# Optimization experiments

Measured on AMD Instinct MI355X. Metric: run time of the kernel, lower is better.

The kernel has to match this reference:

```python
import jax, jax.numpy as jnp
import numpy as np

DIM = 384
NUM_HEADS = 12
WS = 7
POSMLP_DIM = 32
HEAD_DIM = DIM // NUM_HEADS
SCALE = HEAD_DIM ** -0.5


def setup_inputs() -> dict:
    key = jax.random.key(0)
    ks = jax.random.split(key, 10)
    B_ = 2048
    N = WS * WS
    nW = 64
    inp = {
        "x": jax.random.normal(ks[0], (B_, N, DIM), dtype=jnp.float32),
        "mask": jax.random.normal(ks[1], (nW, N, N), dtype=jnp.float32),
        # qkv Linear: weight [3*dim, dim], bias [3*dim]
        "qkv_w": jax.random.normal(ks[2], (3 * DIM, DIM), dtype=jnp.float32) * (DIM ** -0.5),
        "qkv_b": jax.random.normal(ks[3], (3 * DIM,), dtype=jnp.float32) * 0.02,
        # proj Linear
        "proj_w": jax.random.normal(ks[4], (DIM, DIM), dtype=jnp.float32) * (DIM ** -0.5),
        "proj_b": jax.random.normal(ks[5], (DIM,), dtype=jnp.float32) * 0.02,
        # posmlp: Conv2d(2, posmlp_dim, 1) -> ReLU -> Conv2d(posmlp_dim, num_heads, 1)
        "pm_w1": jax.random.normal(ks[6], (POSMLP_DIM, 2), dtype=jnp.float32) * 0.5,
        "pm_b1": jax.random.normal(ks[7], (POSMLP_DIM,), dtype=jnp.float32) * 0.02,
        "pm_w2": jax.random.normal(ks[8], (NUM_HEADS, POSMLP_DIM), dtype=jnp.float32) * (POSMLP_DIM ** -0.5),
        "pm_b2": jax.random.normal(ks[9], (NUM_HEADS,), dtype=jnp.float32) * 0.02,
    }
    return inp


def _pos_bias(pm_w1, pm_b1, pm_w2, pm_b2):
    # pos_hw: [2, N] with channel 0 = row index, channel 1 = col index
    coords = jnp.arange(WS, dtype=jnp.float32)
    pos_h = jnp.repeat(coords[:, None], WS, axis=1).reshape(-1)  # row idx
    pos_w = jnp.tile(coords[None, :], (WS, 1)).reshape(-1)       # col idx
    pos = jnp.stack([pos_h, pos_w], axis=0)                      # [2, N]
    # pos_input[c, i, j] = pos[c, j] - pos[c, i]  (unsqueeze(2) - unsqueeze(3))
    d = pos[:, None, :] - pos[:, :, None]                        # [2, N, N]
    d = jnp.sign(d) * jnp.log1p(jnp.abs(d))
    # 1x1 convs == per-position channel MLP
    h = jax.nn.relu(jnp.einsum("cij,oc->oij", d, pm_w1) + pm_b1[:, None, None])
    bias = jnp.einsum("cij,oc->oij", h, pm_w2) + pm_b2[:, None, None]  # [H, N, N]
    return bias


def reference(x, mask, qkv_w, qkv_b, proj_w, proj_b, pm_w1, pm_b1, pm_w2, pm_b2):
    B_, N, C = x.shape
    H = NUM_HEADS
    qkv = x @ qkv_w.T + qkv_b                                     # [B_, N, 3C]
    qkv = qkv.reshape(B_, N, 3, H, C // H).transpose(2, 0, 3, 1, 4)
    q, k, v = qkv[0], qkv[1], qkv[2]                              # [B_, H, N, d]
    attn = jnp.einsum("bhnd,bhmd->bhnm", q * SCALE, k)            # [B_, H, N, N]
    attn = attn + _pos_bias(pm_w1, pm_b1, pm_w2, pm_b2)[None]
    nW = mask.shape[0]
    attn = attn.reshape(B_ // nW, nW, H, N, N) + mask[None, :, None]
    attn = jax.nn.softmax(attn.reshape(B_, H, N, N), axis=-1)
    out = jnp.einsum("bhnm,bhmd->bhnd", attn, v)                  # [B_, H, N, d]
    out = out.transpose(0, 2, 1, 3).reshape(B_, N, C)
    return out @ proj_w.T + proj_b
```

## Files before the change

kernel.cpp:

```cpp
#include <hip/hip_runtime.h>
#include <hip/hip_bf16.h>
#include <stdint.h>

#define DIM 384
#define QKVN 1152
#define NHEAD 12
#define HDIM 32
#define NTOK 49
#define NWIN 2048
static constexpr float SCALE_Q = 0.17677669529663687f;

typedef float f32x4 __attribute__((ext_vector_type(4)));
typedef float f32x4u __attribute__((ext_vector_type(4), aligned(4)));
typedef __bf16 bf16x8 __attribute__((ext_vector_type(8)));
typedef unsigned short u16;
typedef u16 u16x8 __attribute__((ext_vector_type(8)));
typedef u16 u16x4 __attribute__((ext_vector_type(4)));

static __device__ __forceinline__ u16 f2bf(float f) {
  __hip_bfloat16 h = __float2bfloat16(f);
  return __builtin_bit_cast(unsigned short, h);
}
static __device__ __forceinline__ f32x4 mfma_bf16(u16x8 a, u16x8 b, f32x4 c) {
  return __builtin_amdgcn_mfma_f32_16x16x32_bf16(
      __builtin_bit_cast(bf16x8, a), __builtin_bit_cast(bf16x8, b), c, 0, 0, 0);
}

__global__ void k_convert(const float* __restrict__ s, u16* __restrict__ d, int n) {
  int i = (blockIdx.x * 256 + threadIdx.x) * 4;
  if (i < n) {
    f32x4 v = *(const f32x4*)(s + i);
    u16x4 o;
    o[0] = f2bf(v[0]); o[1] = f2bf(v[1]); o[2] = f2bf(v[2]); o[3] = f2bf(v[3]);
    *(u16x4*)(d + i) = o;
  }
}

__global__ void k_posbias(const float* __restrict__ w1, const float* __restrict__ b1,
                          const float* __restrict__ w2, const float* __restrict__ b2,
                          float* __restrict__ out) {
  int idx = blockIdx.x * 256 + threadIdx.x;
  if (idx >= NTOK * NTOK) return;
  int i = idx / NTOK, j = idx % NTOK;
  float d0 = (float)(j / 7 - i / 7);
  float d1 = (float)(j % 7 - i % 7);
  d0 = copysignf(log1pf(fabsf(d0)), d0);
  d1 = copysignf(log1pf(fabsf(d1)), d1);
  float acc[NHEAD];
#pragma unroll
  for (int o2 = 0; o2 < NHEAD; o2++) acc[o2] = b2[o2];
#pragma unroll 4
  for (int o = 0; o < 32; o++) {
    float h = fmaxf(d0 * w1[o * 2] + d1 * w1[o * 2 + 1] + b1[o], 0.f);
#pragma unroll
    for (int o2 = 0; o2 < NHEAD; o2++) acc[o2] += h * w2[o2 * 32 + o];
  }
#pragma unroll
  for (int o2 = 0; o2 < NHEAD; o2++) out[(o2 * NTOK + i) * NTOK + j] = acc[o2];
}

__global__ void k_pbm(const float* __restrict__ posb, const float* __restrict__ mask,
                      float* __restrict__ pbm) {
  int idx = blockIdx.x * 256 + threadIdx.x;
  if (idx >= 64 * NHEAD * NTOK * NTOK) return;
  int j = idx % (NTOK * NTOK);
  int t = idx / (NTOK * NTOK);
  int h = t % NHEAD, w = t / NHEAD;
  pbm[idx] = posb[h * NTOK * NTOK + j] + mask[w * NTOK * NTOK + j];
}

template <int MODE>
static __device__ __forceinline__ void gemm_body(const void* __restrict__ Ap,
                                                 const u16* __restrict__ Bw,
                                                 const float* __restrict__ bias,
                                                 void* __restrict__ Cp) {
  __shared__ u16 As[2][128 * 64];
  __shared__ u16 Bs[2][128 * 64];
  const int tid = threadIdx.x;
  const int NB = (MODE == 0) ? 9 : 3;
  const int PER = (MODE == 0) ? 882 : 294;
  const int g = blockIdx.x;
  const int flat = (g & 7) * PER + (g >> 3);
  const int bm = flat / NB, bn = flat % NB;

  const int lane = tid & 63, wv = tid >> 6;
  const int wr = wv >> 1, wc = wv & 1;
  const int l15 = lane & 15, l4 = lane >> 4;
  const int sr = tid >> 1, hp = tid & 1;

  const float* a0 = (const float*)Ap + (size_t)(bm * 128 + sr) * DIM + hp * 32;
  const u16*   a1 = (const u16*)Ap + (size_t)(bm * 128 + sr) * DIM + hp * 32;
  const u16*   bb = Bw + (size_t)(bn * 128 + sr) * DIM + hp * 32;

  f32x4 fA[8];
  u16x8 rA[4], rB[4];

#define GLOAD(K0)                                                        \
  {                                                                      \
    if (MODE == 0) {                                                     \
      _Pragma("unroll") for (int i = 0; i < 8; i++)                      \
          fA[i] = *(const f32x4*)(a0 + (K0) + i * 4);                    \
    } else {                                                             \
      _Pragma("unroll") for (int i = 0; i < 4; i++)                      \
          rA[i] = *(const u16x8*)(a1 + (K0) + i * 8);                    \
    }                                                                    \
    _Pragma("unroll") for (int i = 0; i < 4; i++)                        \
        rB[i] = *(const u16x8*)(bb + (K0) + i * 8);                      \
  }

#define WLDS(BUF)                                                        \
  {                                                                      \
    _Pragma("unroll") for (int s = 0; s < 4; s++) {                      \
      u16x8 av;                                                          \
      if (MODE == 0) {                                                   \
        _Pragma("unroll") for (int j = 0; j < 4; j++) {                  \
          av[j] = f2bf(fA[2 * s][j]);                                    \
          av[j + 4] = f2bf(fA[2 * s + 1][j]);                            \
        }                                                                \
      } else av = rA[s];                                                 \
      const int st = ((hp * 4 + s) ^ (sr & 7)) * 8;                      \
      *(u16x8*)&As[BUF][sr * 64 + st] = av;                              \
      *(u16x8*)&Bs[BUF][sr * 64 + st] = rB[s];                           \
    }                                                                    \
  }

  GLOAD(0)
  WLDS(0)
  f32x4 acc[4][4] = {};

  for (int it = 0; it < 6; ++it) {
    const int cur = it & 1;
    if (it < 5) GLOAD((it + 1) * 64)
    __syncthreads();
#pragma unroll
    for (int kk = 0; kk < 2; ++kk) {
      u16x8 af[4], bfr[4];
#pragma unroll
      for (int m = 0; m < 4; m++) {
        const int row = wr * 64 + m * 16 + l15;
        af[m] = *(const u16x8*)&As[cur][row * 64 + (((kk * 4 + l4) ^ (l15 & 7)) * 8)];
      }
#pragma unroll
      for (int n = 0; n < 4; n++) {
        const int row = wc * 64 + n * 16 + l15;
        bfr[n] = *(const u16x8*)&Bs[cur][row * 64 + (((kk * 4 + l4) ^ (l15 & 7)) * 8)];
      }
#pragma unroll
      for (int m = 0; m < 4; m++)
#pragma unroll
        for (int n = 0; n < 4; n++)
          acc[m][n] = mfma_bf16(af[m], bfr[n], acc[m][n]);
    }
    if (it < 5) WLDS(cur ^ 1)
  }
#undef GLOAD
#undef WLDS

#pragma unroll
  for (int n = 0; n < 4; n++) {
    const int col = bn * 128 + wc * 64 + n * 16 + l15;
    const float bv = bias[col];
#pragma unroll
    for (int m = 0; m < 4; m++) {
      const int row0 = bm * 128 + wr * 64 + m * 16 + l4 * 4;
#pragma unroll
      for (int r = 0; r < 4; r++) {
        float v = acc[m][n][r] + bv;
        if (MODE == 0) {
          if (col < DIM) v *= SCALE_Q;
          ((u16*)Cp)[(size_t)(row0 + r) * QKVN + col] = f2bf(v);
        } else {
          ((float*)Cp)[(size_t)(row0 + r) * DIM + col] = v;
        }
      }
    }
  }
}

__global__ __launch_bounds__(256, 2) void k_qkv(const float* __restrict__ Ap,
                                                const u16* __restrict__ Bw,
                                                const float* __restrict__ bias,
                                                u16* __restrict__ Cp) {
  gemm_body<0>(Ap, Bw, bias, Cp);
}
__global__ __launch_bounds__(256, 2) void k_proj(const u16* __restrict__ Ap,
                                                 const u16* __restrict__ Bw,
                                                 const float* __restrict__ bias,
                                                 float* __restrict__ Cp) {
  gemm_body<1>(Ap, Bw, bias, Cp);
}

__global__ __launch_bounds__(256) void k_attn(const u16* __restrict__ qkv,
                                              const float* __restrict__ pbm,
                                              u16* __restrict__ aout) {
  __shared__ u16 qs[2][64 * 32];
  __shared__ u16 ks[2][64 * 32];
  __shared__ u16 vts[2][32 * 72];
  __shared__ float pbs[2][49 * 52 + 16];
  __shared__ u16 ps[64 * 72];
  const int g = blockIdx.x;
  const int b = (((g >> 3) >> 3) << 6) + (g & 7) * 8 + ((g >> 3) & 7);
  const int w = b & 63;
  const int tid = threadIdx.x;
  const int lane = tid & 63, wv = tid >> 6;
  const int l15 = lane & 15, l4 = lane >> 4;
  const int fr = (l15 >> 1) & 3;

  for (int i = tid; i < 64 * 32; i += 256)
    if ((i >> 5) >= NTOK) { qs[0][i] = 0; qs[1][i] = 0; ks[0][i] = 0; ks[1][i] = 0; }
  for (int i = tid; i < 32 * 72; i += 256)
    if ((i % 72) >= NTOK) { vts[0][i] = 0; vts[1][i] = 0; }

  const int trow = tid >> 2, tseg = tid & 3;
  const int fT = (trow >> 1) & 3;
  u16x8 rq, rk, rv;

  int psrc[3], pdst[3];
  bool pvld[3];
#pragma unroll
  for (int j = 0; j < 3; j++) {
    const int i = tid + j * 256;
    pvld[j] = i < 637;
    const int r = pvld[j] ? (i / 13) : 0;
    const int c = pvld[j] ? (i - r * 13) : 0;
    psrc[j] = r * 49 + c * 4;
    pdst[j] = r * 52 + c * 4;
  }
  f32x4u pb[3];

#define LOAD_REGS(h)                                                                 \
  {                                                                                  \
    if (tid < 196) {                                                                 \
      const u16* src = qkv + (size_t)(b * NTOK + trow) * QKVN + (h) * HDIM + tseg * 8; \
      rq = *(const u16x8*)src;                                                       \
      rk = *(const u16x8*)(src + DIM);                                               \
      rv = *(const u16x8*)(src + 2 * DIM);                                           \
    }                                                                                \
    const float* pbase = pbm + (size_t)(w * NHEAD + (h)) * (NTOK * NTOK);            \
    _Pragma("unroll") for (int j = 0; j < 3; j++)                                    \
        if (pvld[j]) pb[j] = *(const f32x4u*)(pbase + psrc[j]);                      \
  }
#define WRITE_LDS(buf)                                                               \
  {                                                                                  \
    if (tid < 196) {                                                                 \
      *(u16x8*)&qs[buf][trow * 32 + (tseg ^ fT) * 8] = rq;                           \
      *(u16x8*)&ks[buf][trow * 32 + (tseg ^ fT) * 8] = rk;                           \
      _Pragma("unroll") for (int j = 0; j < 8; j++)                                  \
          vts[buf][(tseg * 8 + j) * 72 + trow] = rv[j];                              \
    }                                                                                \
    _Pragma("unroll") for (int j = 0; j < 3; j++)                                    \
        if (pvld[j]) *(f32x4*)&pbs[buf][pdst[j]] = pb[j];                            \
  }

  LOAD_REGS(0)
  WRITE_LDS(0)

  const int qrow = wv * 16 + l15;
  const int qc = (qrow < NTOK) ? qrow : NTOK - 1;

  for (int h = 0; h < NHEAD; ++h) {
    const int buf = h & 1;
    if (h + 1 < NHEAD) LOAD_REGS(h + 1)
    __syncthreads();

    u16x8 bq = *(const u16x8*)&qs[buf][(wv * 16 + l15) * 32 + (l4 ^ fr) * 8];
    f32x4 s[4];
#pragma unroll
    for (int n = 0; n < 4; n++) {
      u16x8 ak = *(const u16x8*)&ks[buf][(n * 16 + l15) * 32 + (l4 ^ fr) * 8];
      f32x4 z = {0.f, 0.f, 0.f, 0.f};
      s[n] = mfma_bf16(ak, bq, z);
    }

    const float* pl = &pbs[buf][qc * 52];
    float sv[4][4];
    float mx = -1e30f;
#pragma unroll
    for (int n = 0; n < 4; n++) {
      f32x4 p4 = *(const f32x4*)(pl + n * 16 + l4 * 4);
#pragma unroll
      for (int r = 0; r < 4; r++) {
        const int k = n * 16 + l4 * 4 + r;
        float v = (k < NTOK) ? s[n][r] + p4[r] : -1e30f;
        sv[n][r] = v;
        mx = fmaxf(mx, v);
      }
    }
    mx = fmaxf(mx, __shfl_xor(mx, 16));
    mx = fmaxf(mx, __shfl_xor(mx, 32));
    float e[4][4], sum = 0.f;
#pragma unroll
    for (int n = 0; n < 4; n++)
#pragma unroll
      for (int r = 0; r < 4; r++) {
        const int k = n * 16 + l4 * 4 + r;
        e[n][r] = (k < NTOK) ? __expf(sv[n][r] - mx) : 0.f;
        sum += e[n][r];
      }
    sum += __shfl_xor(sum, 16);
    sum += __shfl_xor(sum, 32);
    const float inv = 1.0f / sum;
#pragma unroll
    for (int n = 0; n < 4; n++) {
      u16x4 pk;
#pragma unroll
      for (int r = 0; r < 4; r++) pk[r] = f2bf(e[n][r] * inv);
      *(u16x4*)&ps[qrow * 72 + n * 16 + l4 * 4] = pk;
    }

    f32x4 o[2] = {};
#pragma unroll
    for (int kk = 0; kk < 2; kk++) {
      u16x8 ap = *(const u16x8*)&ps[(wv * 16 + l15) * 72 + kk * 32 + l4 * 8];
#pragma unroll
      for (int n = 0; n < 2; n++) {
        u16x8 bvv = *(const u16x8*)&vts[buf][(n * 16 + l15) * 72 + kk * 32 + l4 * 8];
        o[n] = mfma_bf16(ap, bvv, o[n]);
      }
    }
#pragma unroll
    for (int n = 0; n < 2; n++) {
      const int col = n * 16 + l15;
#pragma unroll
      for (int r = 0; r < 4; r++) {
        const int row = wv * 16 + l4 * 4 + r;
        if (row < NTOK)
          aout[(size_t)(b * NTOK + row) * DIM + h * HDIM + col] = f2bf(o[n][r]);
      }
    }
    if (h + 1 < NHEAD) WRITE_LDS(buf ^ 1)
  }
#undef LOAD_REGS
#undef WRITE_LDS
}

extern "C" void kernel_launch(void* const* d_in, const int* in_sizes, int n_in,
                              void* d_out, int out_size, void* d_ws, size_t ws_size,
                              hipStream_t stream) {
  const float* x      = (const float*)d_in[0];
  const float* mask   = (const float*)d_in[1];
  const float* qkv_w  = (const float*)d_in[2];
  const float* qkv_b  = (const float*)d_in[3];
  const float* proj_w = (const float*)d_in[4];
  const float* proj_b = (const float*)d_in[5];
  const float* pm_w1  = (const float*)d_in[6];
  const float* pm_b1  = (const float*)d_in[7];
  const float* pm_w2  = (const float*)d_in[8];
  const float* pm_b2  = (const float*)d_in[9];
  float* out = (float*)d_out;

  char* ws = (char*)d_ws;
  u16*   qkv   = (u16*)(ws + 0);
  u16*   wqkv  = (u16*)(ws + 231211008);
  u16*   wproj = (u16*)(ws + 232095744);
  float* posb  = (float*)(ws + 232390656);
  float* pbm   = (float*)(ws + 232505904);
  u16*   aout  = (u16*)(ws + 239881776);

  k_convert<<<432, 256, 0, stream>>>(qkv_w, wqkv, 442368);
  k_convert<<<144, 256, 0, stream>>>(proj_w, wproj, 147456);
  k_posbias<<<10, 256, 0, stream>>>(pm_w1, pm_b1, pm_w2, pm_b2, posb);
  k_pbm<<<7203, 256, 0, stream>>>(posb, mask, pbm);
  k_qkv<<<7056, 256, 0, stream>>>(x, wqkv, qkv_b, qkv);
  k_attn<<<2048, 256, 0, stream>>>(qkv, pbm, aout);
  k_proj<<<2352, 256, 0, stream>>>(aout, wproj, proj_b, out);
}
```

Baseline: 670.0 us.

## Halve GEMM K-tile with folded LDS layout to allow four blocks per CU

Shrinks the shared QKV/proj GEMM K-step from 64 to 32, which halves the LDS buffers and the per-thread staging registers. The 128x32 A and B tiles are folded into 64-row LDS arrays, with the upper half of the rows stored in the second group of swizzled column chunks. Each warp row or column then reads its own chunk group. Launch bounds rise from 2 to 4 blocks per CU to raise occupancy and hide latency, at the cost of twice as many barrier-separated iterations and a tighter register budget.

After: 783.6 us. +17.0%, slower.

```diff
diff --git a/kernel.cpp b/kernel.cpp
--- a/kernel.cpp
+++ b/kernel.cpp
@@ -74,8 +74,8 @@
                                                  const u16* __restrict__ Bw,
                                                  const float* __restrict__ bias,
                                                  void* __restrict__ Cp) {
-  __shared__ u16 As[2][128 * 64];
-  __shared__ u16 Bs[2][128 * 64];
+  __shared__ u16 As[2][64 * 64];
+  __shared__ u16 Bs[2][64 * 64];
   const int tid = threadIdx.x;
   const int NB = (MODE == 0) ? 9 : 3;
   const int PER = (MODE == 0) ? 882 : 294;
@@ -88,70 +88,69 @@
   const int l15 = lane & 15, l4 = lane >> 4;
   const int sr = tid >> 1, hp = tid & 1;
 
-  const float* a0 = (const float*)Ap + (size_t)(bm * 128 + sr) * DIM + hp * 32;
-  const u16*   a1 = (const u16*)Ap + (size_t)(bm * 128 + sr) * DIM + hp * 32;
-  const u16*   bb = Bw + (size_t)(bn * 128 + sr) * DIM + hp * 32;
-
-  f32x4 fA[8];
-  u16x8 rA[4], rB[4];
+  const float* a0 = (const float*)Ap + (size_t)(bm * 128 + sr) * DIM + hp * 16;
+  const u16*   a1 = (const u16*)Ap + (size_t)(bm * 128 + sr) * DIM + hp * 16;
+  const u16*   bb = Bw + (size_t)(bn * 128 + sr) * DIM + hp * 16;
+  const int slr = sr & 63, srh = sr >> 6;
+  const int sw0 = ((srh * 4 + hp * 2) ^ (slr & 7)) * 8;
+  const int sw1 = ((srh * 4 + hp * 2 + 1) ^ (slr & 7)) * 8;
+
+  f32x4 fA[4];
+  u16x8 rA[2], rB[2];
 
 #define GLOAD(K0)                                                        \
   {                                                                      \
     if (MODE == 0) {                                                     \
-      _Pragma("unroll") for (int i = 0; i < 8; i++)                      \
+      _Pragma("unroll") for (int i = 0; i < 4; i++)                      \
           fA[i] = *(const f32x4*)(a0 + (K0) + i * 4);                    \
     } else {                                                             \
-      _Pragma("unroll") for (int i = 0; i < 4; i++)                      \
+      _Pragma("unroll") for (int i = 0; i < 2; i++)                      \
           rA[i] = *(const u16x8*)(a1 + (K0) + i * 8);                    \
     }                                                                    \
-    _Pragma("unroll") for (int i = 0; i < 4; i++)                        \
+    _Pragma("unroll") for (int i = 0; i < 2; i++)                        \
         rB[i] = *(const u16x8*)(bb + (K0) + i * 8);                      \
   }
 
 #define WLDS(BUF)                                                        \
   {                                                                      \
-    _Pragma("unroll") for (int s = 0; s < 4; s++) {                      \
-      u16x8 av;                                                          \
-      if (MODE == 0) {                                                   \
-        _Pragma("unroll") for (int j = 0; j < 4; j++) {                  \
-          av[j] = f2bf(fA[2 * s][j]);                                    \
-          av[j + 4] = f2bf(fA[2 * s + 1][j]);                            \
-        }                                                                \
-      } else av = rA[s];                                                 \
-      const int st = ((hp * 4 + s) ^ (sr & 7)) * 8;                      \
-      *(u16x8*)&As[BUF][sr * 64 + st] = av;                              \
-      *(u16x8*)&Bs[BUF][sr * 64 + st] = rB[s];                           \
-    }                                                                    \
+    u16x8 av0, av1;                                                      \
+    if (MODE == 0) {                                                     \
+      _Pragma("unroll") for (int j = 0; j < 4; j++) {                    \
+        av0[j] = f2bf(fA[0][j]); av0[j + 4] = f2bf(fA[1][j]);            \
+        av1[j] = f2bf(fA[2][j]); av1[j + 4] = f2bf(fA[3][j]);            \
+      }                                                                  \
+    } else { av0 = rA[0]; av1 = rA[1]; }                                 \
+    *(u16x8*)&As[BUF][slr * 64 + sw0] = av0;                             \
+    *(u16x8*)&As[BUF][slr * 64 + sw1] = av1;                             \
+    *(u16x8*)&Bs[BUF][slr * 64 + sw0] = rB[0];                           \
+    *(u16x8*)&Bs[BUF][slr * 64 + sw1] = rB[1];                           \
   }
 
   GLOAD(0)
   WLDS(0)
   f32x4 acc[4][4] = {};
 
-  for (int it = 0; it < 6; ++it) {
+  for (int it = 0; it < 12; ++it) {
     const int cur = it & 1;
-    if (it < 5) GLOAD((it + 1) * 64)
+    if (it < 11) GLOAD((it + 1) * 32)
     __syncthreads();
-#pragma unroll
-    for (int kk = 0; kk < 2; ++kk) {
-      u16x8 af[4], bfr[4];
-#pragma unroll
-      for (int m = 0; m < 4; m++) {
-        const int row = wr * 64 + m * 16 + l15;
-        af[m] = *(const u16x8*)&As[cur][row * 64 + (((kk * 4 + l4) ^ (l15 & 7)) * 8)];
-      }
-#pragma unroll
-      for (int n = 0; n < 4; n++) {
-        const int row = wc * 64 + n * 16 + l15;
-        bfr[n] = *(const u16x8*)&Bs[cur][row * 64 + (((kk * 4 + l4) ^ (l15 & 7)) * 8)];
-      }
-#pragma unroll
-      for (int m = 0; m < 4; m++)
-#pragma unroll
-        for (int n = 0; n < 4; n++)
-          acc[m][n] = mfma_bf16(af[m], bfr[n], acc[m][n]);
-    }
-    if (it < 5) WLDS(cur ^ 1)
+    u16x8 af[4], bfr[4];
+#pragma unroll
+    for (int m = 0; m < 4; m++) {
+      const int lrow = m * 16 + l15;
+      af[m] = *(const u16x8*)&As[cur][lrow * 64 + (((wr * 4 + l4) ^ (lrow & 7)) * 8)];
+    }
+#pragma unroll
+    for (int n = 0; n < 4; n++) {
+      const int lrow = n * 16 + l15;
+      bfr[n] = *(const u16x8*)&Bs[cur][lrow * 64 + (((wc * 4 + l4) ^ (lrow & 7)) * 8)];
+    }
+#pragma unroll
+    for (int m = 0; m < 4; m++)
+#pragma unroll
+      for (int n = 0; n < 4; n++)
+        acc[m][n] = mfma_bf16(af[m], bfr[n], acc[m][n]);
+    if (it < 11) WLDS(cur ^ 1)
   }
 #undef GLOAD
 #undef WLDS
@@ -177,13 +176,13 @@
   }
 }
 
-__global__ __launch_bounds__(256, 2) void k_qkv(const float* __restrict__ Ap,
+__global__ __launch_bounds__(256, 4) void k_qkv(const float* __restrict__ Ap,
                                                 const u16* __restrict__ Bw,
                                                 const float* __restrict__ bias,
                                                 u16* __restrict__ Cp) {
   gemm_body<0>(Ap, Bw, bias, Cp);
 }
-__global__ __launch_bounds__(256, 2) void k_proj(const u16* __restrict__ Ap,
+__global__ __launch_bounds__(256, 4) void k_proj(const u16* __restrict__ Ap,
                                                  const u16* __restrict__ Bw,
                                                  const float* __restrict__ bias,
                                                  float* __restrict__ Cp) {
```
